# Optimization experiments

Measured on AMD Instinct MI355X. Metric: run time of the kernel, lower is better.

Reference implementation:

```python
import jax, jax.numpy as jnp
import numpy as np

EPS = 1e-12

def setup_inputs() -> dict:
    key = jax.random.key(0)
    k1, k2, k3, k4, k5, k6 = jax.random.split(key, 6)
    B, DIM, T = 16, 256, 2048
    K, D = 1024, 64  # num_embeddings, embedding_dim
    N = B * T
    input_data = jax.random.normal(k1, (B, DIM, T), dtype=jnp.float32)
    codebooks = jax.random.normal(k2, (K, D), dtype=jnp.float32)
    W_in = jax.random.normal(k3, (DIM, D), dtype=jnp.float32) / np.sqrt(DIM)
    b_in = jnp.zeros((D,), dtype=jnp.float32)
    W_out = jax.random.normal(k4, (D, DIM), dtype=jnp.float32) / np.sqrt(D)
    b_out = jnp.zeros((DIM,), dtype=jnp.float32)
    random_vector = jax.random.normal(k5, (N, D), dtype=jnp.float32)
    return {"input_data": input_data, "codebooks": codebooks,
            "W_in": W_in, "b_in": b_in, "W_out": W_out, "b_out": b_out,
            "random_vector": random_vector}

def reference(input_data, codebooks, W_in, b_in, W_out, b_out, random_vector):
    B, DIM, T = input_data.shape
    D = codebooks.shape[1]
    # encode: [B, DIM, T] -> [B, T, DIM] -> project -> [B*T, D]
    x = jnp.einsum('bct,cd->btd', input_data, W_in) + b_in
    x = x.reshape(-1, D)  # [N, D]
    distances = (jnp.sum(x * x, axis=1, keepdims=True)
                 - 2.0 * (x @ codebooks.T)
                 + jnp.sum(codebooks * codebooks, axis=1)[None, :])  # [N, K]
    min_indices = jnp.argmin(distances, axis=1)  # [N]
    hard = codebooks[min_indices]  # [N, D]
    # noise substitution
    norm_resid = jnp.sqrt(jnp.sum((x - hard) ** 2, axis=1, keepdims=True))
    norm_rand = jnp.sqrt(jnp.sum(random_vector ** 2, axis=1, keepdims=True))
    vq_error = (norm_resid / (norm_rand + EPS)) * random_vector
    q = x + vq_error  # [N, D]
    # decode: [N, D] -> [B, T, D] -> project_out -> [B, DIM, T]
    q = q.reshape(B, T, D)
    out = jnp.einsum('btd,dc->bct', q, W_out) + b_out[None, :, None]
    return out
```

## Files before the change

### kernel.cpp

```cpp
#include <hip/hip_runtime.h>
#include <hip/hip_bf16.h>

typedef __bf16 bf16x8 __attribute__((ext_vector_type(8)));
typedef unsigned short u16x8 __attribute__((ext_vector_type(8)));
typedef unsigned short u16x4 __attribute__((ext_vector_type(4)));
typedef float f32x4 __attribute__((ext_vector_type(4)));

constexpr int DIMc = 256, Tt = 2048, Kk = 1024, Dd = 64;

__device__ __forceinline__ unsigned short f2b(float f) {
  unsigned u = __float_as_uint(f);
  return (unsigned short)((u + 0x7FFFu + ((u >> 16) & 1u)) >> 16);
}
__device__ __forceinline__ float b2f(unsigned short v) {
  return __uint_as_float(((unsigned)v) << 16);
}
__device__ __forceinline__ f32x4 mfma16(u16x8 a, u16x8 b, f32x4 c) {
  return __builtin_amdgcn_mfma_f32_16x16x32_bf16(
      __builtin_bit_cast(bf16x8, a), __builtin_bit_cast(bf16x8, b), c, 0, 0, 0);
}
__device__ __forceinline__ int ix256(int r, int c) {
  return r * 256 + ((((c >> 3) ^ (r & 7)) << 3) | (c & 7));
}
__device__ __forceinline__ int ix64(int r, int c) {
  return r * 64 + ((((c >> 3) ^ (r & 7)) << 3) | (c & 7));
}

__global__ void nsvq_prep(const float* __restrict__ cb, float* __restrict__ cnorm) {
  int k = blockIdx.x * 256 + threadIdx.x;
  float s = 0.f;
  #pragma unroll
  for (int d = 0; d < Dd; ++d) { float v = cb[(size_t)k * Dd + d]; s = fmaf(v, v, s); }
  cnorm[k] = s;
}

__global__ __launch_bounds__(256, 2) void nsvq_mfma(
    const float* __restrict__ in, const float* __restrict__ rnd,
    const float* __restrict__ cb, const float* __restrict__ Win,
    const float* __restrict__ bin, const float* __restrict__ Wout,
    const float* __restrict__ bout, const float* __restrict__ cnorm,
    float* __restrict__ out) {
  __shared__ unsigned short regA[64 * 256];
  __shared__ unsigned short regB[64 * 256];
  __shared__ unsigned short Xt[64 * 64];
  __shared__ float cnS[128];
  __shared__ float rr2S[64];
  __shared__ float binS[64];
  __shared__ float boutS[256];

  const int tid  = threadIdx.x;
  const int lane = tid & 63;
  const int w    = tid >> 6;
  const int quad = lane >> 4;
  const int col  = lane & 15;
  const int b  = blockIdx.x >> 5;
  const int t0 = (blockIdx.x & 31) << 6;

  for (int i = tid; i < 16384; i += 256) {
    int c = i >> 6, d = i & 63;
    regA[ix256(d, c)] = f2b(Win[i]);
  }
  const float* inb = in + (size_t)b * DIMc * Tt + t0;
  for (int c = (tid >> 6); c < DIMc; c += 4) {
    regB[ix256(lane, c)] = f2b(inb[(size_t)c * Tt + lane]);
  }
  if (tid < 64)  binS[tid]  = bin[tid];
  if (tid < 256) boutS[tid] = bout[tid];

  const float* rb = rnd + (size_t)(b * Tt + t0) * Dd;
  float rv[16];
  #pragma unroll
  for (int tt = 0; tt < 16; ++tt) {
    float v = rb[(size_t)(w * 16 + tt) * Dd + lane];
    rv[tt] = v;
    float s = v * v;
    s += __shfl_xor(s, 1);  s += __shfl_xor(s, 2);  s += __shfl_xor(s, 4);
    s += __shfl_xor(s, 8);  s += __shfl_xor(s, 16); s += __shfl_xor(s, 32);
    if (lane == 0) rr2S[w * 16 + tt] = s;
  }
  __syncthreads();

  u16x8 Bf[8];
  #pragma unroll
  for (int kt = 0; kt < 8; ++kt)
    Bf[kt] = *(const u16x8*)(regB + ix256(w * 16 + col, kt * 32 + quad * 8));
  f32x4 acc[4];
  #pragma unroll
  for (int mt = 0; mt < 4; ++mt) {
    #pragma unroll
    for (int r = 0; r < 4; ++r) acc[mt][r] = binS[mt * 16 + quad * 4 + r];
    #pragma unroll
    for (int kt = 0; kt < 8; ++kt) {
      u16x8 Af = *(const u16x8*)(regA + ix256(mt * 16 + col, kt * 32 + quad * 8));
      acc[mt] = mfma16(Af, Bf[kt], acc[mt]);
    }
  }
  float x2v = 0.f;
  #pragma unroll
  for (int mt = 0; mt < 4; ++mt) {
    u16x4 pk;
    #pragma unroll
    for (int r = 0; r < 4; ++r) {
      x2v = fmaf(acc[mt][r], acc[mt][r], x2v);
      pk[r] = f2b(acc[mt][r]);
    }
    *(u16x4*)(Xt + ix64(w * 16 + col, mt * 16 + quad * 4)) = pk;
  }
  x2v += __shfl_xor(x2v, 16);
  x2v += __shfl_xor(x2v, 32);
  __syncthreads();

  for (int i = tid; i < 16384; i += 256) {
    int d = i >> 8, c = i & 255;
    regB[ix64(c, d)] = f2b(Wout[i]);
  }

  u16x8 Xf[2];
  #pragma unroll
  for (int kt = 0; kt < 2; ++kt)
    Xf[kt] = *(const u16x8*)(Xt + ix64(w * 16 + col, kt * 32 + quad * 8));
  float minv = 3.4e38f;
  for (int ch = 0; ch < 8; ++ch) {
    __syncthreads();
    for (int i = tid; i < 8192; i += 256) {
      int k = i >> 6, d = i & 63;
      regA[ix64(k, d)] = f2b(cb[(size_t)ch * 8192 + i]);
    }
    if (tid < 128) cnS[tid] = cnorm[ch * 128 + tid];
    __syncthreads();
    #pragma unroll
    for (int m = 0; m < 8; ++m) {
      f32x4 a = {0.f, 0.f, 0.f, 0.f};
      u16x8 A0 = *(const u16x8*)(regA + ix64(m * 16 + col, quad * 8));
      u16x8 A1 = *(const u16x8*)(regA + ix64(m * 16 + col, 32 + quad * 8));
      a = mfma16(A0, Xf[0], a);
      a = mfma16(A1, Xf[1], a);
      #pragma unroll
      for (int r = 0; r < 4; ++r)
        minv = fminf(minv, fmaf(-2.f, a[r], cnS[m * 16 + quad * 4 + r]));
    }
  }
  minv = fminf(minv, __shfl_xor(minv, 16));
  minv = fminf(minv, __shfl_xor(minv, 32));

  float r2  = fmaxf(x2v + minv, 0.f);
  float scv = sqrtf(r2) / (sqrtf(rr2S[w * 16 + col]) + 1e-12f);
  #pragma unroll
  for (int tt = 0; tt < 16; ++tt) {
    float s = __shfl(scv, tt);
    int idx = ix64(w * 16 + tt, lane);
    Xt[idx] = f2b(fmaf(s, rv[tt], b2f(Xt[idx])));
  }

  u16x8 Qf0 = *(const u16x8*)(Xt + ix64(w * 16 + col, quad * 8));
  u16x8 Qf1 = *(const u16x8*)(Xt + ix64(w * 16 + col, 32 + quad * 8));
  float* ob0 = out + (size_t)b * DIMc * Tt + t0 + w * 16 + col;
  #pragma unroll
  for (int mt = 0; mt < 16; ++mt) {
    f32x4 a;
    #pragma unroll
    for (int r = 0; r < 4; ++r) a[r] = boutS[mt * 16 + quad * 4 + r];
    u16x8 A0 = *(const u16x8*)(regB + ix64(mt * 16 + col, quad * 8));
    u16x8 A1 = *(const u16x8*)(regB + ix64(mt * 16 + col, 32 + quad * 8));
    a = mfma16(A0, Qf0, a);
    a = mfma16(A1, Qf1, a);
    float* ob = ob0 + (size_t)(mt * 16 + quad * 4) * Tt;
    #pragma unroll
    for (int r = 0; r < 4; ++r) ob[(size_t)r * Tt] = a[r];
  }
}

extern "C" void kernel_launch(void* const* d_in, const int* in_sizes, int n_in,
                              void* d_out, int out_size, void* d_ws, size_t ws_size,
                              hipStream_t stream) {
  const float *in = nullptr, *cb = nullptr, *rnd = nullptr, *bin = nullptr, *bout = nullptr;
  const float* w16[2] = {nullptr, nullptr}; int nw = 0;
  for (int i = 0; i < n_in; ++i) {
    switch (in_sizes[i]) {
      case 8388608: in  = (const float*)d_in[i]; break;
      case 65536:   cb  = (const float*)d_in[i]; break;
      case 2097152: rnd = (const float*)d_in[i]; break;
      case 64:      bin = (const float*)d_in[i]; break;
      case 256:     bout= (const float*)d_in[i]; break;
      case 16384:   if (nw < 2) w16[nw++] = (const float*)d_in[i]; break;
      default: break;
    }
  }
  if (!in)  in  = (const float*)d_in[0];
  if (!cb)  cb  = (const float*)d_in[1];
  if (nw < 2) { w16[0] = (const float*)d_in[2]; w16[1] = (const float*)d_in[4]; }
  if (!bin) bin = (const float*)d_in[3];
  if (!bout) bout = (const float*)d_in[5];
  if (!rnd) rnd = (const float*)d_in[6];
  const float* Win  = w16[0];
  const float* Wout = w16[1];

  float* cnorm = (float*)d_ws;
  float* outp  = (float*)d_out;

  nsvq_prep<<<4, 256, 0, stream>>>(cb, cnorm);
  nsvq_mfma<<<512, 256, 0, stream>>>(in, rnd, cb, Win, bin, Wout, bout, cnorm, outp);
}
```

Baseline: 138.9 us.

## Pre-convert weights to bf16 in workspace, DMA to LDS, and double the token tile

The prep kernel now converts W_in, the codebook (pre-scaled by -2, with its norm folded in as extra columns), and W_out into padded bf16 workspace layouts. Biases and codebook norms are folded into an extra MFMA against a ones vector. The main kernel processes 128 tokens per 512-thread block and loads weights with global_load_lds DMA instead of per-element fp32 conversion. Each weight tile is reused across eight token subtiles, with a cross-wave min reduction through shared memory. This removes redundant per-block fp32 to bf16 conversion and the scalar norm additions, at the cost of more LDS per block and the bf16 hi/lo split precision for the norms.

```diff
diff --git a/kernel.cpp b/kernel.cpp
--- a/kernel.cpp
+++ b/kernel.cpp
@@ -5,94 +5,139 @@
 typedef unsigned short u16x8 __attribute__((ext_vector_type(8)));
 typedef unsigned short u16x4 __attribute__((ext_vector_type(4)));
 typedef float f32x4 __attribute__((ext_vector_type(4)));
+typedef unsigned short u16;
 
 constexpr int DIMc = 256, Tt = 2048, Kk = 1024, Dd = 64;
 
-__device__ __forceinline__ unsigned short f2b(float f) {
+#define WS_WINT 0
+#define WS_CBX  18432
+#define WS_WOX  116736
+
+__device__ __forceinline__ u16 f2b(float f) {
   unsigned u = __float_as_uint(f);
-  return (unsigned short)((u + 0x7FFFu + ((u >> 16) & 1u)) >> 16);
-}
-__device__ __forceinline__ float b2f(unsigned short v) {
+  return (u16)((u + 0x7FFFu + ((u >> 16) & 1u)) >> 16);
+}
+__device__ __forceinline__ float b2f(u16 v) {
   return __uint_as_float(((unsigned)v) << 16);
 }
 __device__ __forceinline__ f32x4 mfma16(u16x8 a, u16x8 b, f32x4 c) {
   return __builtin_amdgcn_mfma_f32_16x16x32_bf16(
       __builtin_bit_cast(bf16x8, a), __builtin_bit_cast(bf16x8, b), c, 0, 0, 0);
 }
-__device__ __forceinline__ int ix256(int r, int c) {
-  return r * 256 + ((((c >> 3) ^ (r & 7)) << 3) | (c & 7));
-}
-__device__ __forceinline__ int ix64(int r, int c) {
-  return r * 64 + ((((c >> 3) ^ (r & 7)) << 3) | (c & 7));
-}
-
-__global__ void nsvq_prep(const float* __restrict__ cb, float* __restrict__ cnorm) {
-  int k = blockIdx.x * 256 + threadIdx.x;
-  float s = 0.f;
-  #pragma unroll
-  for (int d = 0; d < Dd; ++d) { float v = cb[(size_t)k * Dd + d]; s = fmaf(v, v, s); }
-  cnorm[k] = s;
-}
-
-__global__ __launch_bounds__(256, 2) void nsvq_mfma(
+__device__ __forceinline__ void dma16(const u16* g, u16* l) {
+  __builtin_amdgcn_global_load_lds(
+      (const __attribute__((address_space(1))) unsigned int*)g,
+      (__attribute__((address_space(3))) unsigned int*)l, 16, 0, 0);
+}
+
+__global__ void nsvq_prep(const float* __restrict__ cb, const float* __restrict__ Win,
+                          const float* __restrict__ bin, const float* __restrict__ Wout,
+                          const float* __restrict__ bout, u16* __restrict__ wsu) {
+  const int g = blockIdx.x * 256 + threadIdx.x;
+  u16* WinT = wsu + WS_WINT;
+  u16* CbX  = wsu + WS_CBX;
+  u16* WoX  = wsu + WS_WOX;
+  for (int i = g; i < 16384; i += 8192) {
+    int c = i >> 6, d = i & 63;
+    WinT[d * 288 + c] = f2b(Win[i]);
+  }
+  if (g < 2048) {
+    int d = g >> 5, j = g & 31; u16 v = 0;
+    float bv = bin[d]; u16 h = f2b(bv);
+    if (j == 0) v = h; else if (j == 1) v = f2b(bv - b2f(h));
+    WinT[d * 288 + 256 + j] = v;
+  }
+  if (g < 1024) {
+    const float4* cr = (const float4*)(cb + (size_t)g * 64);
+    float vb[64]; float cn = 0.f;
+    #pragma unroll
+    for (int q = 0; q < 16; ++q) {
+      float4 v = cr[q];
+      vb[q*4] = v.x; vb[q*4+1] = v.y; vb[q*4+2] = v.z; vb[q*4+3] = v.w;
+      cn = fmaf(v.x, v.x, fmaf(v.y, v.y, fmaf(v.z, v.z, fmaf(v.w, v.w, cn))));
+    }
+    u16* row = CbX + g * 96;
+    #pragma unroll
+    for (int d = 0; d < 64; ++d) row[d] = f2b(-2.f * vb[d]);
+    u16 h = f2b(cn);
+    row[64] = h; row[65] = f2b(cn - b2f(h));
+    for (int j = 66; j < 96; ++j) row[j] = 0;
+  }
+  for (int i = g; i < 16384; i += 8192) {
+    int d = i >> 8, c = i & 255;
+    WoX[c * 96 + d] = f2b(Wout[i]);
+  }
+  {
+    int c = g >> 5, j = g & 31; u16 v = 0;
+    float bv = bout[c]; u16 h = f2b(bv);
+    if (j == 0) v = h; else if (j == 1) v = f2b(bv - b2f(h));
+    WoX[c * 96 + 64 + j] = v;
+  }
+}
+
+__global__ __launch_bounds__(512, 2) void nsvq_main(
     const float* __restrict__ in, const float* __restrict__ rnd,
-    const float* __restrict__ cb, const float* __restrict__ Win,
-    const float* __restrict__ bin, const float* __restrict__ Wout,
-    const float* __restrict__ bout, const float* __restrict__ cnorm,
-    float* __restrict__ out) {
-  __shared__ unsigned short regA[64 * 256];
-  __shared__ unsigned short regB[64 * 256];
-  __shared__ unsigned short Xt[64 * 64];
-  __shared__ float cnS[128];
-  __shared__ float rr2S[64];
-  __shared__ float binS[64];
-  __shared__ float boutS[256];
-
-  const int tid  = threadIdx.x;
+    const u16* __restrict__ wsu, float* __restrict__ out) {
+  __shared__ u16 buf[24576];
+  __shared__ u16 InT[128 * 256];
+  __shared__ u16 Xt[128 * 64];
+  __shared__ float mnp[8][128];
+
+  const int tid = threadIdx.x;
   const int lane = tid & 63;
-  const int w    = tid >> 6;
-  const int quad = lane >> 4;
-  const int col  = lane & 15;
-  const int b  = blockIdx.x >> 5;
-  const int t0 = (blockIdx.x & 31) << 6;
-
-  for (int i = tid; i < 16384; i += 256) {
-    int c = i >> 6, d = i & 63;
-    regA[ix256(d, c)] = f2b(Win[i]);
-  }
-  const float* inb = in + (size_t)b * DIMc * Tt + t0;
-  for (int c = (tid >> 6); c < DIMc; c += 4) {
-    regB[ix256(lane, c)] = f2b(inb[(size_t)c * Tt + lane]);
-  }
-  if (tid < 64)  binS[tid]  = bin[tid];
-  if (tid < 256) boutS[tid] = bout[tid];
-
-  const float* rb = rnd + (size_t)(b * Tt + t0) * Dd;
-  float rv[16];
+  const int w = tid >> 6;
+  const int quad = lane >> 4, col = lane & 15;
+  const int b  = blockIdx.x >> 4;
+  const int t0 = (blockIdx.x & 15) << 7;
+  const int myt = w * 16 + col;
+
+  {
+    const int t = tid & 127, cg = tid >> 7;
+    const float* ib = in + (size_t)b * DIMc * Tt + t0 + t;
+    #pragma unroll
+    for (int it = 0; it < 8; ++it) {
+      int c0 = cg * 8 + it * 32;
+      u16x8 pk;
+      #pragma unroll
+      for (int j = 0; j < 8; ++j) pk[j] = f2b(ib[(size_t)(c0 + j) * Tt]);
+      *(u16x8*)(InT + t * 256 + ((((c0 >> 3)) ^ (t & 7)) << 3)) = pk;
+    }
+  }
+  #pragma unroll
+  for (int ii = 0; ii < 5; ++ii) {
+    int i = w + 8 * ii;
+    if (i < 36) dma16(wsu + WS_WINT + i * 512 + lane * 8, buf + i * 512);
+  }
+  float rr2v = 0.f;
+  const float* rb = rnd + ((size_t)b * Tt + t0) * Dd;
   #pragma unroll
   for (int tt = 0; tt < 16; ++tt) {
     float v = rb[(size_t)(w * 16 + tt) * Dd + lane];
-    rv[tt] = v;
     float s = v * v;
     s += __shfl_xor(s, 1);  s += __shfl_xor(s, 2);  s += __shfl_xor(s, 4);
     s += __shfl_xor(s, 8);  s += __shfl_xor(s, 16); s += __shfl_xor(s, 32);
-    if (lane == 0) rr2S[w * 16 + tt] = s;
-  }
-  __syncthreads();
-
-  u16x8 Bf[8];
-  #pragma unroll
-  for (int kt = 0; kt < 8; ++kt)
-    Bf[kt] = *(const u16x8*)(regB + ix256(w * 16 + col, kt * 32 + quad * 8));
+    if (col == tt) rr2v = s;
+  }
+  __syncthreads();
+
+  u16x8 Bc1 = {0, 0, 0, 0, 0, 0, 0, 0};
+  if (quad == 0) { Bc1[0] = 0x3F80; Bc1[1] = 0x3F80; }
   f32x4 acc[4];
-  #pragma unroll
-  for (int mt = 0; mt < 4; ++mt) {
-    #pragma unroll
-    for (int r = 0; r < 4; ++r) acc[mt][r] = binS[mt * 16 + quad * 4 + r];
-    #pragma unroll
-    for (int kt = 0; kt < 8; ++kt) {
-      u16x8 Af = *(const u16x8*)(regA + ix256(mt * 16 + col, kt * 32 + quad * 8));
-      acc[mt] = mfma16(Af, Bf[kt], acc[mt]);
+  {
+    u16x8 Bf[8];
+    #pragma unroll
+    for (int kt = 0; kt < 8; ++kt)
+      Bf[kt] = *(const u16x8*)(InT + myt * 256 + (((kt * 4 + quad) ^ (myt & 7)) << 3));
+    #pragma unroll
+    for (int mt = 0; mt < 4; ++mt) {
+      f32x4 a = {0.f, 0.f, 0.f, 0.f};
+      #pragma unroll
+      for (int kt = 0; kt < 8; ++kt) {
+        u16x8 A = *(const u16x8*)(buf + (mt * 16 + col) * 288 + kt * 32 + quad * 8);
+        a = mfma16(A, Bf[kt], a);
+      }
+      u16x8 A8 = *(const u16x8*)(buf + (mt * 16 + col) * 288 + 256 + quad * 8);
+      acc[mt] = mfma16(A8, Bc1, a);
     }
   }
   float x2v = 0.f;
@@ -100,70 +145,91 @@
   for (int mt = 0; mt < 4; ++mt) {
     u16x4 pk;
     #pragma unroll
-    for (int r = 0; r < 4; ++r) {
-      x2v = fmaf(acc[mt][r], acc[mt][r], x2v);
-      pk[r] = f2b(acc[mt][r]);
-    }
-    *(u16x4*)(Xt + ix64(w * 16 + col, mt * 16 + quad * 4)) = pk;
+    for (int r = 0; r < 4; ++r) { x2v = fmaf(acc[mt][r], acc[mt][r], x2v); pk[r] = f2b(acc[mt][r]); }
+    int bk = mt * 2 + (quad >> 1);
+    *(u16x4*)(Xt + myt * 64 + ((bk ^ (myt & 7)) << 3) + (quad & 1) * 4) = pk;
   }
   x2v += __shfl_xor(x2v, 16);
   x2v += __shfl_xor(x2v, 32);
   __syncthreads();
 
-  for (int i = tid; i < 16384; i += 256) {
-    int d = i >> 8, c = i & 255;
-    regB[ix64(c, d)] = f2b(Wout[i]);
-  }
-
-  u16x8 Xf[2];
-  #pragma unroll
-  for (int kt = 0; kt < 2; ++kt)
-    Xf[kt] = *(const u16x8*)(Xt + ix64(w * 16 + col, kt * 32 + quad * 8));
-  float minv = 3.4e38f;
-  for (int ch = 0; ch < 8; ++ch) {
+  u16x8 Xa[8], Xb[8];
+  #pragma unroll
+  for (int nt = 0; nt < 8; ++nt) {
+    int tr = nt * 16 + col;
+    Xa[nt] = *(const u16x8*)(Xt + tr * 64 + ((quad ^ (tr & 7)) << 3));
+    Xb[nt] = *(const u16x8*)(Xt + tr * 64 + (((4 + quad) ^ (tr & 7)) << 3));
+  }
+  float minv[8];
+  #pragma unroll
+  for (int i = 0; i < 8; ++i) minv[i] = 3.4e38f;
+  for (int ch = 0; ch < 4; ++ch) {
+    if (ch) __syncthreads();
+    #pragma unroll
+    for (int ii = 0; ii < 6; ++ii) {
+      int i = w + 8 * ii;
+      dma16(wsu + WS_CBX + ch * 24576 + i * 512 + lane * 8, buf + i * 512);
+    }
     __syncthreads();
-    for (int i = tid; i < 8192; i += 256) {
-      int k = i >> 6, d = i & 63;
-      regA[ix64(k, d)] = f2b(cb[(size_t)ch * 8192 + i]);
-    }
-    if (tid < 128) cnS[tid] = cnorm[ch * 128 + tid];
-    __syncthreads();
-    #pragma unroll
-    for (int m = 0; m < 8; ++m) {
-      f32x4 a = {0.f, 0.f, 0.f, 0.f};
-      u16x8 A0 = *(const u16x8*)(regA + ix64(m * 16 + col, quad * 8));
-      u16x8 A1 = *(const u16x8*)(regA + ix64(m * 16 + col, 32 + quad * 8));
-      a = mfma16(A0, Xf[0], a);
-      a = mfma16(A1, Xf[1], a);
+    #pragma unroll
+    for (int ms = 0; ms < 2; ++ms) {
+      const u16* ar = buf + (w * 32 + ms * 16 + col) * 96;
+      u16x8 A0 = *(const u16x8*)(ar + quad * 8);
+      u16x8 A1 = *(const u16x8*)(ar + 32 + quad * 8);
+      u16x8 A2 = *(const u16x8*)(ar + 64 + quad * 8);
       #pragma unroll
-      for (int r = 0; r < 4; ++r)
-        minv = fminf(minv, fmaf(-2.f, a[r], cnS[m * 16 + quad * 4 + r]));
-    }
-  }
-  minv = fminf(minv, __shfl_xor(minv, 16));
-  minv = fminf(minv, __shfl_xor(minv, 32));
-
-  float r2  = fmaxf(x2v + minv, 0.f);
-  float scv = sqrtf(r2) / (sqrtf(rr2S[w * 16 + col]) + 1e-12f);
+      for (int nt = 0; nt < 8; ++nt) {
+        f32x4 a = {0.f, 0.f, 0.f, 0.f};
+        a = mfma16(A0, Xa[nt], a);
+        a = mfma16(A1, Xb[nt], a);
+        a = mfma16(A2, Bc1, a);
+        #pragma unroll
+        for (int r = 0; r < 4; ++r) minv[nt] = fminf(minv[nt], a[r]);
+      }
+    }
+  }
+  #pragma unroll
+  for (int nt = 0; nt < 8; ++nt) {
+    float m = minv[nt];
+    m = fminf(m, __shfl_xor(m, 16));
+    m = fminf(m, __shfl_xor(m, 32));
+    mnp[w][nt * 16 + col] = m;
+  }
+  __syncthreads();
+
+  #pragma unroll
+  for (int ii = 0; ii < 6; ++ii) {
+    int i = w + 8 * ii;
+    dma16(wsu + WS_WOX + i * 512 + lane * 8, buf + i * 512);
+  }
+  float mv = 3.4e38f;
+  #pragma unroll
+  for (int j = 0; j < 8; ++j) mv = fminf(mv, mnp[j][myt]);
+  float r2  = fmaxf(x2v + mv, 0.f);
+  float scv = sqrtf(r2) / (sqrtf(rr2v) + 1e-12f);
   #pragma unroll
   for (int tt = 0; tt < 16; ++tt) {
     float s = __shfl(scv, tt);
-    int idx = ix64(w * 16 + tt, lane);
-    Xt[idx] = f2b(fmaf(s, rv[tt], b2f(Xt[idx])));
-  }
-
-  u16x8 Qf0 = *(const u16x8*)(Xt + ix64(w * 16 + col, quad * 8));
-  u16x8 Qf1 = *(const u16x8*)(Xt + ix64(w * 16 + col, 32 + quad * 8));
-  float* ob0 = out + (size_t)b * DIMc * Tt + t0 + w * 16 + col;
+    float rv = rb[(size_t)(w * 16 + tt) * Dd + lane];
+    int tr = w * 16 + tt;
+    int idx = tr * 64 + (((lane >> 3) ^ (tr & 7)) << 3) + (lane & 7);
+    Xt[idx] = f2b(fmaf(s, rv, b2f(Xt[idx])));
+  }
+  __syncthreads();
+
+  u16x8 Q0 = *(const u16x8*)(Xt + myt * 64 + ((quad ^ (myt & 7)) << 3));
+  u16x8 Q1 = *(const u16x8*)(Xt + myt * 64 + (((4 + quad) ^ (myt & 7)) << 3));
+  float* ob0 = out + (size_t)b * DIMc * Tt + t0 + myt;
   #pragma unroll
   for (int mt = 0; mt < 16; ++mt) {
-    f32x4 a;
-    #pragma unroll
-    for (int r = 0; r < 4; ++r) a[r] = boutS[mt * 16 + quad * 4 + r];
-    u16x8 A0 = *(const u16x8*)(regB + ix64(mt * 16 + col, quad * 8));
-    u16x8 A1 = *(const u16x8*)(regB + ix64(mt * 16 + col, 32 + quad * 8));
-    a = mfma16(A0, Qf0, a);
-    a = mfma16(A1, Qf1, a);
+    const u16* ar = buf + (mt * 16 + col) * 96;
+    u16x8 A0 = *(const u16x8*)(ar + quad * 8);
+    u16x8 A1 = *(const u16x8*)(ar + 32 + quad * 8);
+    u16x8 A2 = *(const u16x8*)(ar + 64 + quad * 8);
+    f32x4 a = {0.f, 0.f, 0.f, 0.f};
+    a = mfma16(A0, Q0, a);
+    a = mfma16(A1, Q1, a);
+    a = mfma16(A2, Bc1, a);
     float* ob = ob0 + (size_t)(mt * 16 + quad * 4) * Tt;
     #pragma unroll
     for (int r = 0; r < 4; ++r) ob[(size_t)r * Tt] = a[r];
@@ -192,12 +258,10 @@
   if (!bin) bin = (const float*)d_in[3];
   if (!bout) bout = (const float*)d_in[5];
   if (!rnd) rnd = (const float*)d_in[6];
-  const float* Win  = w16[0];
-  const float* Wout = w16[1];
-
-  float* cnorm = (float*)d_ws;
-  float* outp  = (float*)d_out;
-
-  nsvq_prep<<<4, 256, 0, stream>>>(cb, cnorm);
-  nsvq_mfma<<<512, 256, 0, stream>>>(in, rnd, cb, Win, bin, Wout, bout, cnorm, outp);
-}
+
+  u16* wsu = (u16*)d_ws;
+  float* outp = (float*)d_out;
+
+  nsvq_prep<<<32, 256, 0, stream>>>(cb, w16[0], bin, w16[1], bout, wsu);
+  nsvq_main<<<256, 512, 0, stream>>>(in, rnd, wsu, outp);
+}
```

Measured after the change: 116.0 us. 16.5% less time.
